# Kernel tuning notes

Hardware: AMD Instinct MI355X
Metric: run time of the kernel (lower is better)

Reference implementation:

```python
import jax, jax.numpy as jnp
import numpy as np
from jax import lax

SINKHORN_ITERS = 20
SINKHORN_REG = 0.05
OT_BLUR = 0.05
OT_ITERS = 20
LAMBDA_OT = 0.1
LAMBDA_REG = 0.01
N_SUB = 2048


def pairwise_dist_sq(a, b):
    # a: [B,N,3], b: [B,M,3] -> [B,N,M]
    a_sq = jnp.sum(a * a, axis=-1, keepdims=True)          # [B,N,1]
    b_sq = jnp.sum(b * b, axis=-1, keepdims=True)          # [B,M,1]
    ab = jnp.einsum('bnd,bmd->bnm', a, b)
    return jnp.maximum(a_sq + jnp.swapaxes(b_sq, 1, 2) - 2.0 * ab, 0.0)


def farthest_point_sample(x, n_sub):
    # x: [B,N,3] -> int32 indices [B,n_sub]; sequential min-distance update loop
    B, N, _ = x.shape

    def body(i, state):
        dists, farthest, sel = state
        sel = sel.at[:, i].set(farthest)
        centroid = jnp.take_along_axis(x, farthest[:, None, None], axis=1)  # [B,1,3]
        d = jnp.sum((x - centroid) ** 2, axis=-1)                            # [B,N]
        dists = jnp.minimum(dists, d)
        farthest = jnp.argmax(dists, axis=-1).astype(jnp.int32)
        return dists, farthest, sel

    dists = jnp.full((B, N), jnp.inf, dtype=x.dtype)
    farthest = jnp.zeros((B,), dtype=jnp.int32)
    sel = jnp.zeros((B, n_sub), dtype=jnp.int32)
    _, _, sel = lax.fori_loop(0, n_sub, body, (dists, farthest, sel))
    return sel


def sinkhorn_assignment(cost, n_iters=SINKHORN_ITERS, reg=SINKHORN_REG):
    # log-domain Sinkhorn -> soft doubly-stochastic P [B,N,M]
    log_K = -cost / reg
    B, N, M = cost.shape
    log_u = jnp.zeros((B, N), dtype=cost.dtype)
    log_v = jnp.zeros((B, M), dtype=cost.dtype)

    def body(carry, _):
        lu, lv = carry
        lu = -jax.nn.logsumexp(log_K + lv[:, None, :], axis=2)
        lv = -jax.nn.logsumexp(log_K + lu[:, :, None], axis=1)
        return (lu, lv), None

    (log_u, log_v), _ = lax.scan(body, (log_u, log_v), None, length=n_iters)
    return jnp.exp(log_K + log_u[:, :, None] + log_v[:, None, :])


def _ot_eps(x, y, eps, n_iters=OT_ITERS):
    # balanced entropic OT dual value per batch (geomloss sinkhorn, p=2: C=|x-y|^2/2)
    C = 0.5 * pairwise_dist_sq(x, y)
    B, N, M = C.shape
    log_mu = -jnp.log(jnp.asarray(N, C.dtype))
    log_nu = -jnp.log(jnp.asarray(M, C.dtype))
    f = jnp.zeros((B, N), dtype=C.dtype)
    g = jnp.zeros((B, M), dtype=C.dtype)

    def body(carry, _):
        f, g = carry
        f = -eps * jax.nn.logsumexp((g[:, None, :] - C) / eps + log_nu, axis=2)
        g = -eps * jax.nn.logsumexp((f[:, :, None] - C) / eps + log_mu, axis=1)
        return (f, g), None

    (f, g), _ = lax.scan(body, (f, g), None, length=n_iters)
    return jnp.mean(f, axis=1) + jnp.mean(g, axis=1)  # [B]


def sinkhorn_divergence(x, y, eps):
    return jnp.mean(_ot_eps(x, y, eps) - 0.5 * _ot_eps(x, x, eps) - 0.5 * _ot_eps(y, y, eps))


def _forward(target_sub, idx_dummy, t, template, W_enc, b_enc, W1, b1, W2, b2):
    pass


def setup_inputs() -> dict:
    key = jax.random.key(0)
    ks = jax.random.split(key, 9)
    B, N = 8, 16384
    d_z, d_h = 256, 256
    return {
        'target': jax.random.normal(ks[0], (B, N, 3), dtype=jnp.float32),
        't': jax.random.uniform(ks[1], (B,), dtype=jnp.float32),
        'template': jax.random.normal(ks[2], (N_SUB, 3), dtype=jnp.float32),
        'W_enc': jax.random.normal(ks[3], (3, d_z), dtype=jnp.float32) * 0.05,
        'b_enc': jnp.zeros((d_z,), dtype=jnp.float32),
        'W1': jax.random.normal(ks[4], (3 + 1 + d_z, d_h), dtype=jnp.float32) * 0.05,
        'b1': jnp.zeros((d_h,), dtype=jnp.float32),
        'W2': jax.random.normal(ks[5], (d_h, 3), dtype=jnp.float32) * 0.05,
        'b2': jnp.zeros((3,), dtype=jnp.float32),
    }


def reference(target, t, template, W_enc, b_enc, W1, b1, W2, b2):
    B, N, _ = target.shape
    n_sub = template.shape[0]
    t = jnp.clip(t, 1e-5, 1.0 - 1e-5)

    # FPS subsample target (n_sub < N); template already at n_sub points
    idx = farthest_point_sample(target, n_sub)                        # [B,n_sub]
    target_sub = jnp.take_along_axis(target, idx[:, :, None], axis=1)  # [B,n_sub,3]
    template_sub = jnp.broadcast_to(template[None], (B, n_sub, 3))

    # Sinkhorn OT alignment
    cost = pairwise_dist_sq(template_sub, target_sub)                  # [B,n_sub,n_sub]
    P = sinkhorn_assignment(cost)
    target_perm = jnp.einsum('bnm,bmd->bnd', P, target_sub)

    # straight-line interpolant + gt velocity
    v_gt = target_perm - template_sub
    t_ = t[:, None, None]
    x_t = (1.0 - t_) * template_sub + t_ * target_perm

    # encode (stand-in model): per-point linear + max-pool
    feat = jax.nn.relu(target_sub @ W_enc + b_enc)                     # [B,n_sub,d_z]
    z = jnp.max(feat, axis=1)                                          # [B,d_z]

    # velocity prediction (stand-in MLP conditioned on x_t, t, z)
    h_in = jnp.concatenate([
        x_t,
        jnp.broadcast_to(t_, (B, n_sub, 1)),
        jnp.broadcast_to(z[:, None, :], (B, n_sub, z.shape[-1])),
    ], axis=-1)
    v_pred = jax.nn.relu(h_in @ W1 + b1) @ W2 + b2                      # [B,n_sub,3]

    loss_velocity = jnp.mean((v_pred - v_gt) ** 2)

    # OT loss on x1 approx (no grad through v_pred, matching torch.no_grad)
    x_1_approx = template_sub + lax.stop_gradient(v_pred)
    eps = jnp.asarray(OT_BLUR ** 2, target.dtype)
    loss_ot = sinkhorn_divergence(x_1_approx, target_sub, eps)

    # template regularisation towards unit norm
    template_norms = jnp.sqrt(jnp.sum(template * template, axis=-1))
    loss_reg = jnp.mean((template_norms - 1.0) ** 2)

    loss = loss_velocity + LAMBDA_OT * loss_ot + LAMBDA_REG * loss_reg
    return loss, loss_velocity, loss_ot, loss_reg
```

## Files before the change

kernel.cpp:

```cpp
#include <hip/hip_runtime.h>
#include <math.h>

#define NPTS 16384
#define NB 8
#define NS 2048
#define DZ 256

typedef float v2f __attribute__((ext_vector_type(2)));

#define OFF_SCAL 0
#define OFF_LU   64
#define OFF_LV   (OFF_LU + NB*NS)
#define OFF_F    (OFF_LV + NB*NS)
#define OFF_G    (OFF_F + 3*NB*NS)
#define ZERO_FLOATS (OFF_G + 3*NB*NS)
#define OFF_IDX  ZERO_FLOATS
#define OFF_YP   (OFF_IDX + NB*NS)
#define OFF_TP   (OFF_YP + NB*NS*4)
#define OFF_XP   (OFF_TP + NS*4)
#define OFF_PERM (OFF_XP + NB*NS*4)
#define OFF_Z    (OFF_PERM + NB*NS*3)
#define OFF_HB   (OFF_Z + NB*DZ)

__global__ __launch_bounds__(1024) void fps_kernel(const float* __restrict__ x,
                                                   int* __restrict__ sel){
  #pragma clang fp contract(off)
  const int b = blockIdx.x, tid = threadIdx.x;
  const float* xb = x + (size_t)b * NPTS * 3;
  float c[48];
  {
    const float4* s4 = (const float4*)(xb + (size_t)tid * 48);
    #pragma unroll
    for (int q = 0; q < 12; q++){
      float4 v = s4[q];
      c[4*q] = v.x; c[4*q+1] = v.y; c[4*q+2] = v.z; c[4*q+3] = v.w;
    }
  }
  v2f X[8], Y[8], Z[8], D[8];
  #pragma unroll
  for (int j = 0; j < 8; j++){
    v2f vx = {c[6*j],   c[6*j+3]};
    v2f vy = {c[6*j+1], c[6*j+4]};
    v2f vz = {c[6*j+2], c[6*j+5]};
    v2f vi = {INFINITY, INFINITY};
    X[j] = vx; Y[j] = vy; Z[j] = vz; D[j] = vi;
  }
  __shared__ float sC[3];
  __shared__ int sIdx;
  __shared__ unsigned long long sKey;
  if (tid == 0){ sIdx = 0; sKey = ~0ull; sC[0] = c[0]; sC[1] = c[1]; sC[2] = c[2]; }
  __syncthreads();

  for (int i = 0; i < NS; i++){
    const float c0 = sC[0], c1 = sC[1], c2 = sC[2];
    if (tid == 0) sel[b*NS + i] = sIdx;
    v2f c0v = {c0, c0}, c1v = {c1, c1}, c2v = {c2, c2};
    v2f lm = {-INFINITY, -INFINITY};
    #pragma unroll
    for (int j = 0; j < 8; j++){
      v2f dx = X[j] - c0v;
      v2f dy = Y[j] - c1v;
      v2f dz = Z[j] - c2v;
      v2f d2 = (dx*dx + dy*dy) + dz*dz;
      v2f nd = __builtin_elementwise_min(D[j], d2);
      D[j] = nd;
      lm = __builtin_elementwise_max(lm, nd);
    }
    const float lmaxT = fmaxf(lm.x, lm.y);
    float wmax = lmaxT;
    #pragma unroll
    for (int o = 32; o; o >>= 1) wmax = fmaxf(wmax, __shfl_xor(wmax, o, 64));
    if (lmaxT == wmax){
      int kk = 15;
      #pragma unroll
      for (int j = 7; j >= 0; j--){
        if (D[j].y == lmaxT) kk = 2*j + 1;
        if (D[j].x == lmaxT) kk = 2*j;
      }
      unsigned long long key =
        ((unsigned long long)(~__float_as_uint(lmaxT)) << 32) |
        (unsigned int)(tid*16 + kk);
      atomicMin(&sKey, key);
    }
    __syncthreads();
    const unsigned long long k2 = sKey;
    const int gidx = (int)(k2 & 0xffffffffu);
    if (tid == (gidx >> 4)){
      const int kk = gidx & 15;
      float px = 0.f, py = 0.f, pz = 0.f;
      #pragma unroll
      for (int j = 0; j < 8; j++){
        if (kk == 2*j)   { px = X[j].x; py = Y[j].x; pz = Z[j].x; }
        if (kk == 2*j+1) { px = X[j].y; py = Y[j].y; pz = Z[j].y; }
      }
      sC[0] = px; sC[1] = py; sC[2] = pz;
      sIdx = gidx;
      sKey = ~0ull;
    }
    __syncthreads();
  }
}

__global__ __launch_bounds__(256) void gather_pack_kernel(const float* __restrict__ x,
                                                          const int* __restrict__ sel,
                                                          float4* __restrict__ yp){
  const int b = blockIdx.y;
  const int k = blockIdx.x*256 + threadIdx.x;
  const int p = sel[b*NS + k];
  const float* s = x + ((size_t)b*NPTS + p)*3;
  const float x0 = s[0], x1 = s[1], x2 = s[2];
  const float sq = fmaf(x0,x0, fmaf(x1,x1, x2*x2));
  yp[b*NS + k] = make_float4(x0, x1, x2, sq);
}

__global__ __launch_bounds__(256) void pack_t_kernel(const float* __restrict__ tmpl,
                                                     float4* __restrict__ tp,
                                                     float* __restrict__ sumreg){
  __shared__ float sbuf[4];
  const int k = blockIdx.x*256 + threadIdx.x;
  const float x0 = tmpl[3*k], x1 = tmpl[3*k+1], x2 = tmpl[3*k+2];
  const float sq = fmaf(x0,x0, fmaf(x1,x1, x2*x2));
  tp[k] = make_float4(x0, x1, x2, sq);
  const float n = sqrtf(sq) - 1.0f;
  float v = n*n;
  #pragma unroll
  for (int o = 32; o; o >>= 1) v += __shfl_xor(v, o, 64);
  if ((threadIdx.x & 63) == 0) sbuf[threadIdx.x >> 6] = v;
  __syncthreads();
  if (threadIdx.x == 0){
    float t = 0.f;
    for (int w = 0; w < 4; w++) t += sbuf[w];
    atomicAdd(sumreg, t);
  }
}

__global__ __launch_bounds__(256) void feat_z_kernel(const float4* __restrict__ yp,
                                                     const float* __restrict__ Wenc,
                                                     const float* __restrict__ benc,
                                                     float* __restrict__ z){
  __shared__ float4 sy[NS];
  const int b = blockIdx.x, tid = threadIdx.x;
  for (int j = tid; j < NS; j += 256) sy[j] = yp[b*NS + j];
  __syncthreads();
  const float w0 = Wenc[tid], w1 = Wenc[256+tid], w2 = Wenc[512+tid], bb = benc[tid];
  float m = -INFINITY;
  for (int n = 0; n < NS; n++){
    float4 q = sy[n];
    float v = fmaf(q.x, w0, fmaf(q.y, w1, fmaf(q.z, w2, bb)));
    m = fmaxf(m, fmaxf(v, 0.0f));
  }
  z[b*DZ + tid] = m;
}

__global__ __launch_bounds__(256) void hbase_kernel(const float* __restrict__ z,
                                                    const float* __restrict__ W1,
                                                    const float* __restrict__ b1,
                                                    const float* __restrict__ tarr,
                                                    float* __restrict__ hb){
  __shared__ float sz[DZ];
  const int b = blockIdx.x, cidx = threadIdx.x;
  sz[cidx] = z[b*DZ + cidx];
  __syncthreads();
  const float t = fminf(fmaxf(tarr[b], 1e-5f), (float)(1.0 - 1e-5));
  float acc = fmaf(t, W1[3*256 + cidx], b1[cidx]);
  for (int k = 0; k < DZ; k++) acc = fmaf(sz[k], W1[(4 + k)*256 + cidx], acc);
  hb[b*DZ + cidx] = acc;
}

__device__ __forceinline__ void sink_pass_core(const float4* __restrict__ PI, long piStride,
                                               const float4* __restrict__ PJ, long pjStride,
                                               const float* __restrict__ dIn,
                                               float* __restrict__ dOut,
                                               float H, float twoH, float dMul, float dAdd,
                                               float oScale, float4* S){
  const int tid = threadIdx.x;
  const int b = blockIdx.z;
  {
    const float4* pj = PJ + pjStride*b;
    const float* din = dIn + (size_t)b*NS;
    for (int j = tid; j < NS; j += 1024){
      float4 q = pj[j];
      float E = fmaf(-H, q.w, fmaf(din[j], dMul, dAdd));
      S[j] = make_float4(q.x, q.y, q.z, E);
    }
  }
  __syncthreads();
  const int w = tid >> 6, lane = tid & 63;
  const int i = blockIdx.x*16 + w;
  const float4 pi = PI[piStride*b + i];
  const float R = -H*pi.w;
  float mx = -INFINITY, s = 0.0f;
  #pragma unroll 2
  for (int k = 0; k < 8; k++){
    const int j0 = k*256 + lane;
    float4 a0 = S[j0], a1 = S[j0+64], a2 = S[j0+128], a3 = S[j0+192];
    float v0 = fmaf(twoH, fmaf(pi.x,a0.x, fmaf(pi.y,a0.y, pi.z*a0.z)), a0.w + R);
    float v1 = fmaf(twoH, fmaf(pi.x,a1.x, fmaf(pi.y,a1.y, pi.z*a1.z)), a1.w + R);
    float v2 = fmaf(twoH, fmaf(pi.x,a2.x, fmaf(pi.y,a2.y, pi.z*a2.z)), a2.w + R);
    float v3 = fmaf(twoH, fmaf(pi.x,a3.x, fmaf(pi.y,a3.y, pi.z*a3.z)), a3.w + R);
    float m4 = fmaxf(fmaxf(v0, v1), fmaxf(v2, v3));
    float nm = fmaxf(mx, m4);
    s = fmaf(s, __expf(mx - nm),
             __expf(v0 - nm) + __expf(v1 - nm) + __expf(v2 - nm) + __expf(v3 - nm));
    mx = nm;
  }
  #pragma unroll
  for (int o = 32; o; o >>= 1){
    float om = __shfl_xor(mx, o, 64);
    float os = __shfl_xor(s,  o, 64);
    float nm = fmaxf(mx, om);
    s = fmaf(s, __expf(mx - nm), os*__expf(om - nm));
    mx = nm;
  }
  if (lane == 0) dOut[(size_t)b*NS + i] = oScale*(mx + __logf(s));
}

__global__ __launch_bounds__(1024) void sink_assign_kernel(const float4* __restrict__ tp,
                                                           const float4* __restrict__ yp,
                                                           float* __restrict__ lu,
                                                           float* __restrict__ lv,
                                                           int dir, float H, float twoH){
  __shared__ float4 S[NS];
  if (dir == 0) sink_pass_core(tp, 0,  yp, NS, lv, lu, H, twoH, 1.0f, 0.0f, -1.0f, S);
  else          sink_pass_core(yp, NS, tp, 0,  lu, lv, H, twoH, 1.0f, 0.0f, -1.0f, S);
}

__global__ __launch_bounds__(1024) void sink_ot_kernel(const float4* __restrict__ xp,
                                                       const float4* __restrict__ yp,
                                                       float* __restrict__ F,
                                                       float* __restrict__ G,
                                                       int dir, float H, float twoH,
                                                       float dMul, float dAdd, float oScale){
  __shared__ float4 S[NS];
  const int p = blockIdx.y;
  const float4* first  = (p == 2) ? yp : xp;
  const float4* second = (p == 1) ? xp : yp;
  float* f = F + (size_t)p*NB*NS;
  float* g = G + (size_t)p*NB*NS;
  if (dir == 0) sink_pass_core(first,  NS, second, NS, g, f, H, twoH, dMul, dAdd, oScale, S);
  else          sink_pass_core(second, NS, first,  NS, f, g, H, twoH, dMul, dAdd, oScale, S);
}

__global__ __launch_bounds__(1024) void perm_kernel(const float4* __restrict__ tp,
                                                    const float4* __restrict__ yp,
                                                    const float* __restrict__ lu,
                                                    const float* __restrict__ lv,
                                                    float* __restrict__ perm,
                                                    float H, float twoH){
  __shared__ float4 S[NS];
  const int tid = threadIdx.x, b = blockIdx.z;
  for (int j = tid; j < NS; j += 1024){
    float4 q = yp[(size_t)b*NS + j];
    float E = fmaf(-H, q.w, lv[(size_t)b*NS + j]);
    S[j] = make_float4(q.x, q.y, q.z, E);
  }
  __syncthreads();
  const int w = tid >> 6, lane = tid & 63;
  const int i = blockIdx.x*16 + w;
  const float4 pi = tp[i];
  const float R = fmaf(-H, pi.w, lu[(size_t)b*NS + i]);
  float a0 = 0.f, a1 = 0.f, a2 = 0.f;
  #pragma unroll 2
  for (int k = 0; k < 8; k++){
    #pragma unroll
    for (int u = 0; u < 4; u++){
      const int j = k*256 + u*64 + lane;
      float4 q = S[j];
      float val = fmaf(twoH, fmaf(pi.x,q.x, fmaf(pi.y,q.y, pi.z*q.z)), q.w + R);
      float wgt = __expf(val);
      a0 = fmaf(wgt, q.x, a0);
      a1 = fmaf(wgt, q.y, a1);
      a2 = fmaf(wgt, q.z, a2);
    }
  }
  #pragma unroll
  for (int o = 32; o; o >>= 1){
    a0 += __shfl_xor(a0, o, 64);
    a1 += __shfl_xor(a1, o, 64);
    a2 += __shfl_xor(a2, o, 64);
  }
  if (lane == 0){
    float* d = perm + ((size_t)b*NS + i)*3;
    d[0] = a0; d[1] = a1; d[2] = a2;
  }
}

__global__ __launch_bounds__(128) void mlp_kernel(const float4* __restrict__ tp,
                                                  const float* __restrict__ perm,
                                                  const float* __restrict__ hb,
                                                  const float* __restrict__ W1,
                                                  const float* __restrict__ W2,
                                                  const float* __restrict__ b2,
                                                  const float* __restrict__ tarr,
                                                  float4* __restrict__ xp,
                                                  float* __restrict__ sumvel){
  __shared__ float sw0[256], sw1[256], sw2[256], shb[256], sW2[768];
  __shared__ float sred[2];
  const int tid = threadIdx.x;
  const int r = blockIdx.x*128 + tid;
  const int b = r >> 11, n = r & (NS - 1);
  for (int k = tid; k < 256; k += 128){
    sw0[k] = W1[k]; sw1[k] = W1[256+k]; sw2[k] = W1[512+k]; shb[k] = hb[b*256 + k];
  }
  for (int k = tid; k < 768; k += 128) sW2[k] = W2[k];
  __syncthreads();
  const float t = fminf(fmaxf(tarr[b], 1e-5f), (float)(1.0 - 1e-5));
  const float4 T = tp[n];
  const float pm0 = perm[(size_t)r*3], pm1 = perm[(size_t)r*3+1], pm2 = perm[(size_t)r*3+2];
  const float omt = 1.0f - t;
  const float xt0 = omt*T.x + t*pm0;
  const float xt1 = omt*T.y + t*pm1;
  const float xt2 = omt*T.z + t*pm2;
  float a0 = b2[0], a1 = b2[1], a2 = b2[2];
  for (int cc = 0; cc < 256; cc++){
    float pre = fmaf(xt0, sw0[cc], fmaf(xt1, sw1[cc], fmaf(xt2, sw2[cc], shb[cc])));
    float h = fmaxf(pre, 0.0f);
    a0 = fmaf(h, sW2[3*cc],   a0);
    a1 = fmaf(h, sW2[3*cc+1], a1);
    a2 = fmaf(h, sW2[3*cc+2], a2);
  }
  const float vg0 = pm0 - T.x, vg1 = pm1 - T.y, vg2 = pm2 - T.z;
  const float d0 = a0 - vg0, d1 = a1 - vg1, d2 = a2 - vg2;
  float ls = fmaf(d0,d0, fmaf(d1,d1, d2*d2));
  const float x0 = T.x + a0, x1 = T.y + a1, x2 = T.z + a2;
  const float sq = fmaf(x0,x0, fmaf(x1,x1, x2*x2));
  xp[r] = make_float4(x0, x1, x2, sq);
  #pragma unroll
  for (int o = 32; o; o >>= 1) ls += __shfl_xor(ls, o, 64);
  if ((tid & 63) == 0) sred[tid >> 6] = ls;
  __syncthreads();
  if (tid == 0) atomicAdd(sumvel, sred[0] + sred[1]);
}

__global__ __launch_bounds__(256) void ot_sum_kernel(const float* __restrict__ F,
                                                     const float* __restrict__ G,
                                                     float* __restrict__ ot){
  __shared__ float sbuf[8];
  const int pb = blockIdx.x;
  const float* f = F + (size_t)pb*NS;
  const float* g = G + (size_t)pb*NS;
  float sf = 0.f, sg = 0.f;
  for (int j = threadIdx.x; j < NS; j += 256){ sf += f[j]; sg += g[j]; }
  #pragma unroll
  for (int o = 32; o; o >>= 1){ sf += __shfl_xor(sf, o, 64); sg += __shfl_xor(sg, o, 64); }
  if ((threadIdx.x & 63) == 0){ sbuf[threadIdx.x >> 6] = sf; sbuf[4 + (threadIdx.x >> 6)] = sg; }
  __syncthreads();
  if (threadIdx.x == 0){
    float tf = 0.f, tg = 0.f;
    for (int w = 0; w < 4; w++){ tf += sbuf[w]; tg += sbuf[4 + w]; }
    ot[pb] = tf/(float)NS + tg/(float)NS;
  }
}

__global__ void finalize_kernel(const float* __restrict__ scal, float* __restrict__ out){
  if (threadIdx.x == 0){
    const float* ot = scal + 2;
    float lot = 0.f;
    for (int b = 0; b < NB; b++)
      lot += ot[0*NB + b] - 0.5f*ot[1*NB + b] - 0.5f*ot[2*NB + b];
    lot /= (float)NB;
    const float lvv = scal[0] / (float)(NB*NS*3);
    const float lrg = scal[1] / (float)NS;
    out[0] = lvv + 0.1f*lot + 0.01f*lrg;
    out[1] = lvv;
    out[2] = lot;
    out[3] = lrg;
  }
}

extern "C" void kernel_launch(void* const* d_in, const int* in_sizes, int n_in,
                              void* d_out, int out_size, void* d_ws, size_t ws_size,
                              hipStream_t stream){
  (void)in_sizes; (void)n_in; (void)out_size; (void)ws_size;
  const float* target = (const float*)d_in[0];
  const float* tarr   = (const float*)d_in[1];
  const float* tmpl   = (const float*)d_in[2];
  const float* Wenc   = (const float*)d_in[3];
  const float* benc   = (const float*)d_in[4];
  const float* W1     = (const float*)d_in[5];
  const float* b1     = (const float*)d_in[6];
  const float* W2     = (const float*)d_in[7];
  const float* b2     = (const float*)d_in[8];
  float* out = (float*)d_out;
  float* ws  = (float*)d_ws;

  float*  scal = ws + OFF_SCAL;
  float*  lu   = ws + OFF_LU;
  float*  lv   = ws + OFF_LV;
  float*  F    = ws + OFF_F;
  float*  G    = ws + OFF_G;
  int*    sel  = (int*)(ws + OFF_IDX);
  float4* yp   = (float4*)(ws + OFF_YP);
  float4* tp   = (float4*)(ws + OFF_TP);
  float4* xp   = (float4*)(ws + OFF_XP);
  float*  perm = ws + OFF_PERM;
  float*  z    = ws + OFF_Z;
  float*  hb   = ws + OFF_HB;

  hipMemsetAsync(ws, 0, (size_t)ZERO_FLOATS*sizeof(float), stream);

  fps_kernel<<<NB, 1024, 0, stream>>>(target, sel);
  gather_pack_kernel<<<dim3(8, NB), 256, 0, stream>>>(target, sel, yp);
  pack_t_kernel<<<8, 256, 0, stream>>>(tmpl, tp, scal + 1);
  feat_z_kernel<<<NB, 256, 0, stream>>>(yp, Wenc, benc, z);
  hbase_kernel<<<NB, 256, 0, stream>>>(z, W1, b1, tarr, hb);

  const float INVREG = 1.0f/0.05f;
  for (int it = 0; it < 20; ++it){
    sink_assign_kernel<<<dim3(128,1,NB), 1024, 0, stream>>>(tp, yp, lu, lv, 0, INVREG, 2.0f*INVREG);
    sink_assign_kernel<<<dim3(128,1,NB), 1024, 0, stream>>>(tp, yp, lu, lv, 1, INVREG, 2.0f*INVREG);
  }
  perm_kernel<<<dim3(128,1,NB), 1024, 0, stream>>>(tp, yp, lu, lv, perm, INVREG, 2.0f*INVREG);
  mlp_kernel<<<128, 128, 0, stream>>>(tp, perm, hb, W1, W2, b2, tarr, xp, scal + 0);

  const float EPS    = (float)(0.05*0.05);
  const float INVEPS = 1.0f/EPS;
  const float HOT    = 0.5f*INVEPS;
  const float LOGNU  = (float)(-log(2048.0));
  for (int it = 0; it < 20; ++it){
    sink_ot_kernel<<<dim3(128,3,NB), 1024, 0, stream>>>(xp, yp, F, G, 0, HOT, INVEPS, INVEPS, LOGNU, -EPS);
    sink_ot_kernel<<<dim3(128,3,NB), 1024, 0, stream>>>(xp, yp, F, G, 1, HOT, INVEPS, INVEPS, LOGNU, -EPS);
  }
  ot_sum_kernel<<<24, 256, 0, stream>>>(F, G, scal + 2);
  finalize_kernel<<<1, 64, 0, stream>>>(scal, out);
}
```

Before: 6.832 ms.

## Restructure FPS argmax to one barrier per iteration with double-buffered wave keys

The farthest-point-sampling kernel now runs 512 threads with 32 points each instead of 1024 threads with 16. Each iteration does a wave-level 64-bit key min via shuffles, writes one key per wave into a parity double-buffered shared array, and has every thread reduce the 8 wave keys after a single barrier. Every thread then reloads the chosen centroid from global memory. This removes the shared atomicMin, the second barrier and the owner-thread broadcast from the serial 2048-step loop. The cost is more registers per thread and a global load each iteration whose latency sits on the critical path.

```diff
diff --git a/kernel.cpp b/kernel.cpp
--- a/kernel.cpp
+++ b/kernel.cpp
@@ -22,82 +22,86 @@
 #define OFF_Z    (OFF_PERM + NB*NS*3)
 #define OFF_HB   (OFF_Z + NB*DZ)
 
-__global__ __launch_bounds__(1024) void fps_kernel(const float* __restrict__ x,
-                                                   int* __restrict__ sel){
+__global__ __launch_bounds__(512) void fps_kernel(const float* __restrict__ x,
+                                                  int* __restrict__ sel){
   #pragma clang fp contract(off)
   const int b = blockIdx.x, tid = threadIdx.x;
   const float* xb = x + (size_t)b * NPTS * 3;
-  float c[48];
+  float c[96];
   {
-    const float4* s4 = (const float4*)(xb + (size_t)tid * 48);
-    #pragma unroll
-    for (int q = 0; q < 12; q++){
+    const float4* s4 = (const float4*)(xb + (size_t)tid * 96);
+    #pragma unroll
+    for (int q = 0; q < 24; q++){
       float4 v = s4[q];
       c[4*q] = v.x; c[4*q+1] = v.y; c[4*q+2] = v.z; c[4*q+3] = v.w;
     }
   }
-  v2f X[8], Y[8], Z[8], D[8];
-  #pragma unroll
-  for (int j = 0; j < 8; j++){
-    v2f vx = {c[6*j],   c[6*j+3]};
-    v2f vy = {c[6*j+1], c[6*j+4]};
-    v2f vz = {c[6*j+2], c[6*j+5]};
-    v2f vi = {INFINITY, INFINITY};
-    X[j] = vx; Y[j] = vy; Z[j] = vz; D[j] = vi;
-  }
-  __shared__ float sC[3];
-  __shared__ int sIdx;
-  __shared__ unsigned long long sKey;
-  if (tid == 0){ sIdx = 0; sKey = ~0ull; sC[0] = c[0]; sC[1] = c[1]; sC[2] = c[2]; }
-  __syncthreads();
+  v2f X[16], Y[16], Z[16], D[16];
+  #pragma unroll
+  for (int j = 0; j < 16; j++){
+    X[j] = (v2f){c[6*j],   c[6*j+3]};
+    Y[j] = (v2f){c[6*j+1], c[6*j+4]};
+    Z[j] = (v2f){c[6*j+2], c[6*j+5]};
+    D[j] = (v2f){INFINITY, INFINITY};
+  }
+  __shared__ unsigned long long sK[2][8];
+  float c0 = xb[0], c1 = xb[1], c2 = xb[2];
+  int widx = 0;
+  const int wv = tid >> 6, lane = tid & 63;
 
   for (int i = 0; i < NS; i++){
-    const float c0 = sC[0], c1 = sC[1], c2 = sC[2];
-    if (tid == 0) sel[b*NS + i] = sIdx;
-    v2f c0v = {c0, c0}, c1v = {c1, c1}, c2v = {c2, c2};
-    v2f lm = {-INFINITY, -INFINITY};
-    #pragma unroll
-    for (int j = 0; j < 8; j++){
+    if (tid == 0) sel[b*NS + i] = widx;
+    const v2f c0v = {c0,c0}, c1v = {c1,c1}, c2v = {c2,c2};
+    #pragma unroll
+    for (int j = 0; j < 16; j++){
       v2f dx = X[j] - c0v;
       v2f dy = Y[j] - c1v;
       v2f dz = Z[j] - c2v;
       v2f d2 = (dx*dx + dy*dy) + dz*dz;
-      v2f nd = __builtin_elementwise_min(D[j], d2);
-      D[j] = nd;
-      lm = __builtin_elementwise_max(lm, nd);
-    }
-    const float lmaxT = fmaxf(lm.x, lm.y);
-    float wmax = lmaxT;
-    #pragma unroll
-    for (int o = 32; o; o >>= 1) wmax = fmaxf(wmax, __shfl_xor(wmax, o, 64));
-    if (lmaxT == wmax){
-      int kk = 15;
-      #pragma unroll
-      for (int j = 7; j >= 0; j--){
-        if (D[j].y == lmaxT) kk = 2*j + 1;
-        if (D[j].x == lmaxT) kk = 2*j;
-      }
-      unsigned long long key =
-        ((unsigned long long)(~__float_as_uint(lmaxT)) << 32) |
-        (unsigned int)(tid*16 + kk);
-      atomicMin(&sKey, key);
-    }
+      D[j] = __builtin_elementwise_min(D[j], d2);
+    }
+    v2f m0 = __builtin_elementwise_max(D[0],  D[1]);
+    v2f m1 = __builtin_elementwise_max(D[2],  D[3]);
+    v2f m2 = __builtin_elementwise_max(D[4],  D[5]);
+    v2f m3 = __builtin_elementwise_max(D[6],  D[7]);
+    v2f m4 = __builtin_elementwise_max(D[8],  D[9]);
+    v2f m5 = __builtin_elementwise_max(D[10], D[11]);
+    v2f m6 = __builtin_elementwise_max(D[12], D[13]);
+    v2f m7 = __builtin_elementwise_max(D[14], D[15]);
+    m0 = __builtin_elementwise_max(m0, m1);
+    m2 = __builtin_elementwise_max(m2, m3);
+    m4 = __builtin_elementwise_max(m4, m5);
+    m6 = __builtin_elementwise_max(m6, m7);
+    m0 = __builtin_elementwise_max(m0, m2);
+    m4 = __builtin_elementwise_max(m4, m6);
+    m0 = __builtin_elementwise_max(m0, m4);
+    const float lmax = fmaxf(m0.x, m0.y);
+    int kk = 31;
+    #pragma unroll
+    for (int j = 15; j >= 0; j--){
+      if (D[j].y == lmax) kk = 2*j + 1;
+      if (D[j].x == lmax) kk = 2*j;
+    }
+    unsigned long long key =
+      ((unsigned long long)(~__float_as_uint(lmax)) << 32) |
+      (unsigned int)(tid*32 + kk);
+    #pragma unroll
+    for (int o = 32; o; o >>= 1){
+      unsigned long long ok = __shfl_xor(key, o, 64);
+      key = (ok < key) ? ok : key;
+    }
+    const int par = i & 1;
+    if (lane == 0) sK[par][wv] = key;
     __syncthreads();
-    const unsigned long long k2 = sKey;
-    const int gidx = (int)(k2 & 0xffffffffu);
-    if (tid == (gidx >> 4)){
-      const int kk = gidx & 15;
-      float px = 0.f, py = 0.f, pz = 0.f;
-      #pragma unroll
-      for (int j = 0; j < 8; j++){
-        if (kk == 2*j)   { px = X[j].x; py = Y[j].x; pz = Z[j].x; }
-        if (kk == 2*j+1) { px = X[j].y; py = Y[j].y; pz = Z[j].y; }
-      }
-      sC[0] = px; sC[1] = py; sC[2] = pz;
-      sIdx = gidx;
-      sKey = ~0ull;
-    }
-    __syncthreads();
+    unsigned long long best = sK[par][0];
+    #pragma unroll
+    for (int w = 1; w < 8; w++){
+      unsigned long long k2 = sK[par][w];
+      best = (k2 < best) ? k2 : best;
+    }
+    widx = (int)(best & 0xffffffffu);
+    const float* cp = xb + (size_t)widx * 3;
+    c0 = cp[0]; c1 = cp[1]; c2 = cp[2];
   }
 }
 
@@ -399,7 +403,7 @@
 
   hipMemsetAsync(ws, 0, (size_t)ZERO_FLOATS*sizeof(float), stream);
 
-  fps_kernel<<<NB, 1024, 0, stream>>>(target, sel);
+  fps_kernel<<<NB, 512, 0, stream>>>(target, sel);
   gather_pack_kernel<<<dim3(8, NB), 256, 0, stream>>>(target, sel, yp);
   pack_t_kernel<<<8, 256, 0, stream>>>(tmpl, tp, scal + 1);
   feat_z_kernel<<<NB, 256, 0, stream>>>(yp, Wenc, benc, z);
```

After: 5.748 ms. -15.9%, faster.
